# Kernel tuning notes

Hardware: AMD Instinct MI355X
Metric: run time of the kernel (lower is better)

Reference implementation:

```python
import jax, jax.numpy as jnp
import numpy as np

B, C, H, W = 16, 512, 64, 64
G = 32
CG = C // G       # per-group channels = 16


def setup_inputs() -> dict:
    key = jax.random.key(0)
    ks = jax.random.split(key, 6)
    def w(k, shape, fan_in):
        return (jax.random.normal(k, shape, jnp.float32) / np.float32(np.sqrt(fan_in)))
    return {
        "x": jax.random.normal(ks[0], (B, C, H, W), jnp.float32),
        "conv1_w": w(ks[1], (CG, CG), CG), "conv1_b": jnp.zeros((CG,), jnp.float32),
        "convh_w": w(ks[2], (CG, CG), CG), "convh_b": jnp.zeros((CG,), jnp.float32),
        "convw_w": w(ks[3], (CG, CG), CG), "convw_b": jnp.zeros((CG,), jnp.float32),
        "conv3_w": w(ks[4], (CG, CG, 3, 3), CG * 9), "conv3_b": jnp.zeros((CG,), jnp.float32),
        "gn_w": jnp.ones((CG,), jnp.float32), "gn_b": jnp.zeros((CG,), jnp.float32),
    }


def _conv1x1(y, w, b):
    # y: [N, Ci, L]  w: [Co, Ci]  -> [N, Co, L]
    return jnp.einsum('oi,bil->bol', w, y) + b[None, :, None]


def _ema_forward(x, conv1_w, conv1_b, convh_w, convh_b, convw_w, convw_b,
                 conv3_w, conv3_b, gn_w, gn_b):
    b, c, h, w = x.shape
    g, cg, hw = G, CG, h * w
    bg = b * g
    xg = x.reshape(bg, cg, h, w)

    # coordinate pooling: row means [bg,cg,h], col means [bg,cg,w]
    x_h = xg.mean(axis=3)                     # [bg, cg, h]
    x_w = xg.mean(axis=2)                     # [bg, cg, w]
    y = jnp.concatenate([x_h, x_w], axis=2)   # [bg, cg, h+w]
    y = jax.nn.relu(_conv1x1(y, conv1_w, conv1_b))
    y_h, y_w = y[:, :, :h], y[:, :, h:]

    a_h = jax.nn.sigmoid(_conv1x1(y_h, convh_w, convh_b))[:, :, :, None]  # [bg,cg,h,1]
    a_w = jax.nn.sigmoid(_conv1x1(y_w, convw_w, convw_b))[:, :, None, :]  # [bg,cg,1,w]

    x1 = xg * a_h * a_w

    # GroupNorm(num_groups=1): normalize over (cg,h,w) per sample, affine per channel
    mu = x1.mean(axis=(1, 2, 3), keepdims=True)
    var = ((x1 - mu) ** 2).mean(axis=(1, 2, 3), keepdims=True)
    x2 = (x1 - mu) * jax.lax.rsqrt(var + 1e-5)
    x2 = x2 * gn_w[None, :, None, None] + gn_b[None, :, None, None]

    # 3x3 conv branch
    x3 = jax.lax.conv_general_dilated(
        xg, conv3_w, window_strides=(1, 1), padding='SAME',
        dimension_numbers=('NCHW', 'OIHW', 'NCHW'))
    x3 = jax.nn.relu(x3 + conv3_b[None, :, None, None])

    A2 = jax.nn.softmax(x2.reshape(bg, cg, hw), axis=-1)  # [bg,cg,hw]
    A3 = jax.nn.softmax(x3.reshape(bg, cg, hw), axis=-1)
    V2 = x2.mean(axis=(2, 3))                              # [bg,cg]
    V3 = x3.mean(axis=(2, 3))

    s2 = jnp.einsum('bc,bcl->bl', V2, A3)  # [bg, hw]
    s3 = jnp.einsum('bc,bcl->bl', V3, A2)
    s = jax.nn.softmax(s2 + s3, axis=-1).reshape(bg, 1, h, w)

    return (xg * s).reshape(b, c, h, w)


def reference(x, conv1_w, conv1_b, convh_w, convh_b, convw_w, convw_b,
              conv3_w, conv3_b, gn_w, gn_b):
    return _ema_forward(x, conv1_w, conv1_b, convh_w, convh_b, convw_w, convw_b,
                        conv3_w, conv3_b, gn_w, gn_b)
```

## Files before the change

### kernel.cpp

```cpp
#include <hip/hip_runtime.h>
#include <hip/hip_bf16.h>

#define CHW  65536
#define CHW4 16384

__device__ __forceinline__ float wred(float v){
#pragma unroll
  for (int o = 32; o; o >>= 1) v += __shfl_xor(v, o, 64);
  return v;
}
__device__ __forceinline__ float wred16(float v){
#pragma unroll
  for (int o = 8; o; o >>= 1) v += __shfl_xor(v, o, 64);
  return v;
}
__device__ __forceinline__ float bf2f(unsigned short u){
  return __uint_as_float(((unsigned)u) << 16);
}

#define STR 84
__global__ __launch_bounds__(256, 6) void k3_conv(const float* __restrict__ x,
    const float* __restrict__ w3, const float* __restrict__ b3,
    __hip_bfloat16* __restrict__ E3,
    float* __restrict__ V3part, float* __restrict__ Z3part)
{
  __shared__ __align__(16) float in_s[8*10*STR];
  int tid = threadIdx.x;
  int s   = blockIdx.x;
  int bg  = blockIdx.y;
  size_t base  = (size_t)bg * CHW;
  const float4* x4 = (const float4*)x + (size_t)bg * CHW4;
  int lane = tid & 63;
  int cog = __builtin_amdgcn_readfirstlane(tid >> 6);
  int co0 = cog * 4;
  int r  = lane >> 3;
  int w0 = (lane & 7) * 8;
  float acc[4][8];
#pragma unroll
  for (int i = 0; i < 4; ++i)
#pragma unroll
    for (int px = 0; px < 8; ++px) acc[i][px] = 0.f;

#pragma unroll 1
  for (int half = 0; half < 2; ++half){
    __syncthreads();
    for (int idx = tid; idx < 1440; idx += 256){
      int q   = idx % 18;
      int rr  = (idx / 18) % 10;
      int ci8 = idx / 180;
      int hh  = s*8 - 1 + rr;
      float4 v = make_float4(0.f, 0.f, 0.f, 0.f);
      if (q >= 1 && q <= 16 && (unsigned)hh < 64u)
        v = x4[(half*8 + ci8)*1024 + hh*16 + (q-1)];
      *(float4*)&in_s[(ci8*10 + rr)*STR + q*4] = v;
    }
    __syncthreads();
#pragma unroll 1
    for (int ci8 = 0; ci8 < 8; ++ci8){
      int ci = half*8 + ci8;
      float wgt[4][9];
#pragma unroll
      for (int i = 0; i < 4; ++i)
#pragma unroll
        for (int t = 0; t < 9; ++t)
          wgt[i][t] = w3[((co0+i)*16 + ci)*9 + t];
#pragma unroll
      for (int dy = 0; dy < 3; ++dy){
        const float* row = &in_s[(ci8*10 + r + dy)*STR + w0];
        float4 A0 = *(const float4*)(row);
        float4 A1 = *(const float4*)(row+4);
        float4 A2v = *(const float4*)(row+8);
        float4 A3v = *(const float4*)(row+12);
        float v[16] = {A0.x,A0.y,A0.z,A0.w, A1.x,A1.y,A1.z,A1.w,
                       A2v.x,A2v.y,A2v.z,A2v.w, A3v.x,A3v.y,A3v.z,A3v.w};
#pragma unroll
        for (int dx = 0; dx < 3; ++dx){
#pragma unroll
          for (int px = 0; px < 8; ++px){
            float iv = v[px + dx + 3];
#pragma unroll
            for (int i = 0; i < 4; ++i)
              acc[i][px] = fmaf(wgt[i][dy*3+dx], iv, acc[i][px]);
          }
        }
      }
    }
  }
  int hh = s*8 + r;
#pragma unroll
  for (int i = 0; i < 4; ++i){
    float bias = b3[co0+i];
    union { __hip_bfloat16 hb[8]; uint4 u; } pk;
    float v3acc = 0.f, z3acc = 0.f;
#pragma unroll
    for (int px = 0; px < 8; ++px){
      float val = fmaxf(acc[i][px] + bias, 0.f);
      float e = __expf(val);
      v3acc += val;
      z3acc += e;
      pk.hb[px] = __float2bfloat16(e);
    }
    *(uint4*)&E3[base + (size_t)(co0+i)*4096 + hh*64 + w0] = pk.u;
    float rv = wred(v3acc);
    float rz = wred(z3acc);
    if (lane == 0){
      V3part[((size_t)bg*8 + s)*16 + co0 + i] = rv;
      Z3part[((size_t)bg*8 + s)*16 + co0 + i] = rz;
    }
  }
}

__global__ __launch_bounds__(1024, 8) void mega(const float* __restrict__ x,
    const float* __restrict__ w1, const float* __restrict__ b1,
    const float* __restrict__ wh, const float* __restrict__ bh,
    const float* __restrict__ ww, const float* __restrict__ bw,
    const float* __restrict__ gnw, const float* __restrict__ gnb,
    const float* __restrict__ V3part, const float* __restrict__ Z3part,
    const __hip_bfloat16* __restrict__ E3,
    float* __restrict__ out)
{
  __shared__ float rs[1024];
  __shared__ float cs[1024];
  __shared__ float ym[2048];
  __shared__ __align__(16) float ahs[1024], aws[1024];
  __shared__ float chpart[256], zpart[256];
  __shared__ float red1[16], red2[16];
  __shared__ float murs[2];
  __shared__ float sc_s[16], of_s[16], v2_s[16], p2s[16], p3s[16];
  __shared__ float invS_s;

  int tid = threadIdx.x, bg = blockIdx.x;
  const float4* x4 = (const float4*)x + (size_t)bg * CHW4;
  const ushort4* E34 = (const ushort4*)E3 + (size_t)bg * CHW4;
  float4* o4 = (float4*)out + (size_t)bg * CHW4;
  int h = tid >> 4, w4 = tid & 15, lane = tid & 63, wv = tid >> 6;

  cs[tid] = 0.f;
  __syncthreads();
#pragma unroll 4
  for (int k = 0; k < 16; ++k){
    float4 v = x4[k*1024 + tid];
    float srow = v.x + v.y + v.z + v.w;
    srow = wred16(srow);
    if ((tid & 15) == 0) rs[k*64 + h] = srow;
    v.x += __shfl_xor(v.x, 16); v.x += __shfl_xor(v.x, 32);
    v.y += __shfl_xor(v.y, 16); v.y += __shfl_xor(v.y, 32);
    v.z += __shfl_xor(v.z, 16); v.z += __shfl_xor(v.z, 32);
    v.w += __shfl_xor(v.w, 16); v.w += __shfl_xor(v.w, 32);
    if (lane < 16){
      atomicAdd(&cs[k*64 + lane*4 + 0], v.x);
      atomicAdd(&cs[k*64 + lane*4 + 1], v.y);
      atomicAdd(&cs[k*64 + lane*4 + 2], v.z);
      atomicAdd(&cs[k*64 + lane*4 + 3], v.w);
    }
  }
  __syncthreads();
  for (int ol = tid; ol < 2048; ol += 1024){
    int o = ol >> 7, l = ol & 127;
    float acc = b1[o];
#pragma unroll
    for (int i = 0; i < 16; ++i){
      float mv = (l < 64 ? rs[i*64 + l] : cs[i*64 + (l-64)]) * (1.f/64.f);
      acc = fmaf(w1[o*16 + i], mv, acc);
    }
    ym[o*128 + l] = fmaxf(acc, 0.f);
  }
  __syncthreads();
  for (int ol = tid; ol < 2048; ol += 1024){
    int q = ol >> 10;
    int o = (ol >> 6) & 15;
    int p = ol & 63;
    const float* Wm = q ? ww : wh;
    float acc = q ? bw[o] : bh[o];
#pragma unroll
    for (int i = 0; i < 16; ++i)
      acc = fmaf(Wm[o*16 + i], ym[i*128 + q*64 + p], acc);
    float sg = 1.f / (1.f + __expf(-acc));
    (q ? aws : ahs)[o*64 + p] = sg;
  }
  __syncthreads();

  const float4* aws4 = (const float4*)aws;
  float s1 = 0.f, s2 = 0.f;
#pragma unroll 4
  for (int k = 0; k < 16; ++k){
    float4 v = x4[k*1024 + tid];
    float ah = ahs[k*64 + h];
    float4 aw = aws4[k*16 + w4];
    float4 x1;
    x1.x = v.x * ah * aw.x;
    x1.y = v.y * ah * aw.y;
    x1.z = v.z * ah * aw.z;
    x1.w = v.w * ah * aw.w;
    float csum = x1.x + x1.y + x1.z + x1.w;
    s1 += csum;
    s2 = fmaf(x1.x, x1.x, s2); s2 = fmaf(x1.y, x1.y, s2);
    s2 = fmaf(x1.z, x1.z, s2); s2 = fmaf(x1.w, x1.w, s2);
    float cw = wred(csum);
    if (lane == 0) chpart[k*16 + wv] = cw;
  }
  float r1 = wred(s1), r2 = wred(s2);
  if (lane == 0){ red1[wv] = r1; red2[wv] = r2; }
  __syncthreads();
  if (tid == 0){
    float S = 0.f, SS = 0.f;
#pragma unroll
    for (int i = 0; i < 16; ++i){ S += red1[i]; SS += red2[i]; }
    float mu = S * (1.f/65536.f);
    float var = SS * (1.f/65536.f) - mu*mu;
    murs[0] = mu; murs[1] = rsqrtf(var + 1e-5f);
  }
  __syncthreads();
  if (tid < 16){
    float ch = 0.f;
#pragma unroll
    for (int m = 0; m < 16; ++m) ch += chpart[tid*16 + m];
    float mu = murs[0], rstd = murs[1];
    float g = gnw[tid], b = gnb[tid];
    float sc = rstd * g;
    sc_s[tid] = sc; of_s[tid] = b - mu*sc;
    v2_s[tid] = (ch * (1.f/4096.f) - mu) * sc + b;
  }
  __syncthreads();

#pragma unroll 2
  for (int k = 0; k < 16; ++k){
    float4 v = x4[k*1024 + tid];
    float ah = ahs[k*64 + h];
    float4 aw = aws4[k*16 + w4];
    float sc = sc_s[k], of = of_s[k];
    float z =  __expf(fmaf(v.x * ah * aw.x, sc, of));
    z += __expf(fmaf(v.y * ah * aw.y, sc, of));
    z += __expf(fmaf(v.z * ah * aw.z, sc, of));
    z += __expf(fmaf(v.w * ah * aw.w, sc, of));
    float zw = wred(z);
    if (lane == 0) zpart[k*16 + wv] = zw;
  }
  __syncthreads();
  if (tid < 16){
    float z2 = 0.f;
#pragma unroll
    for (int m = 0; m < 16; ++m) z2 += zpart[tid*16 + m];
    float v3 = 0.f, z3 = 0.f;
#pragma unroll
    for (int ss = 0; ss < 8; ++ss){
      v3 += V3part[((size_t)bg*8 + ss)*16 + tid];
      z3 += Z3part[((size_t)bg*8 + ss)*16 + tid];
    }
    p2s[tid] = v3 * (1.f/4096.f) / z2;
    p3s[tid] = v2_s[tid] / z3;
  }
  __syncthreads();

  float4 tacc = make_float4(0.f,0.f,0.f,0.f);
#pragma unroll 2
  for (int k = 0; k < 16; ++k){
    float4 v = x4[k*1024 + tid];
    ushort4 eu = E34[k*1024 + tid];
    float ah = ahs[k*64 + h];
    float4 aw = aws4[k*16 + w4];
    float sc = sc_s[k], of = of_s[k], p2 = p2s[k], p3 = p3s[k];
    tacc.x += __expf(fmaf(v.x*ah*aw.x, sc, of))*p2 + bf2f(eu.x)*p3;
    tacc.y += __expf(fmaf(v.y*ah*aw.y, sc, of))*p2 + bf2f(eu.y)*p3;
    tacc.z += __expf(fmaf(v.z*ah*aw.z, sc, of))*p2 + bf2f(eu.z)*p3;
    tacc.w += __expf(fmaf(v.w*ah*aw.w, sc, of))*p2 + bf2f(eu.w)*p3;
  }
  float4 e;
  e.x = __expf(tacc.x); e.y = __expf(tacc.y);
  e.z = __expf(tacc.z); e.w = __expf(tacc.w);
  float es = e.x + e.y + e.z + e.w;
  float rr = wred(es);
  if (lane == 0) red1[wv] = rr;
  __syncthreads();
  if (tid == 0){
    float S = 0.f;
#pragma unroll
    for (int i = 0; i < 16; ++i) S += red1[i];
    invS_s = 1.f / S;
  }
  __syncthreads();
  float iS = invS_s;
  float4 ei = make_float4(e.x*iS, e.y*iS, e.z*iS, e.w*iS);

#pragma unroll 4
  for (int k = 0; k < 16; ++k){
    float4 v = x4[k*1024 + tid];
    float4 ov;
    ov.x = v.x * ei.x; ov.y = v.y * ei.y;
    ov.z = v.z * ei.z; ov.w = v.w * ei.w;
    o4[k*1024 + tid] = ov;
  }
}

extern "C" void kernel_launch(void* const* d_in, const int* in_sizes, int n_in,
                              void* d_out, int out_size, void* d_ws, size_t ws_size,
                              hipStream_t stream)
{
  const float* x   = (const float*)d_in[0];
  const float* w1  = (const float*)d_in[1];
  const float* b1  = (const float*)d_in[2];
  const float* wh  = (const float*)d_in[3];
  const float* bh  = (const float*)d_in[4];
  const float* ww  = (const float*)d_in[5];
  const float* bw  = (const float*)d_in[6];
  const float* w3  = (const float*)d_in[7];
  const float* b3  = (const float*)d_in[8];
  const float* gnw = (const float*)d_in[9];
  const float* gnb = (const float*)d_in[10];
  float* out = (float*)d_out;

  float* V3part = (float*)d_ws;
  float* Z3part = V3part + 65536;
  __hip_bfloat16* E3 = (__hip_bfloat16*)(Z3part + 65536);
  (void)ws_size; (void)n_in; (void)in_sizes; (void)out_size;

  k3_conv<<<dim3(8, 512), 256, 0, stream>>>(x, w3, b3, E3, V3part, Z3part);
  mega   <<<512, 1024, 0, stream>>>(x, w1, b1, wh, bh, ww, bw, gnw, gnb,
                                    V3part, Z3part, E3, out);
}
```

Measured before the change: 470.3 us.

## Fuse 3x3 conv into main kernel, keep conv exponentials in shared memory

The separate conv kernel is merged into the per-group kernel. Four 256-thread units each compute two 8-row slabs of the 3x3 conv, prefetching the next slab's inputs into registers while computing the current one. Conv exponentials are stored as bf16 in LDS instead of a global workspace, and the GN-softmax exponentials are cached as packed bf16 in registers so the final pass does not recompute exp or reload x. This removes the global E3 round trip and one kernel launch. In exchange each block uses about 160KB of LDS, so only one block fits per CU, and the grid of 512 blocks gives reduced parallelism for the conv stage.

```diff
diff --git a/kernel.cpp b/kernel.cpp
--- a/kernel.cpp
+++ b/kernel.cpp
@@ -1,8 +1,8 @@
 #include <hip/hip_runtime.h>
 #include <hip/hip_bf16.h>
 
-#define CHW  65536
 #define CHW4 16384
+#define STR  84
 
 __device__ __forceinline__ float wred(float v){
 #pragma unroll
@@ -17,127 +17,159 @@
 __device__ __forceinline__ float bf2f(unsigned short u){
   return __uint_as_float(((unsigned)u) << 16);
 }
-
-#define STR 84
-__global__ __launch_bounds__(256, 6) void k3_conv(const float* __restrict__ x,
-    const float* __restrict__ w3, const float* __restrict__ b3,
-    __hip_bfloat16* __restrict__ E3,
-    float* __restrict__ V3part, float* __restrict__ Z3part)
-{
-  __shared__ __align__(16) float in_s[8*10*STR];
-  int tid = threadIdx.x;
-  int s   = blockIdx.x;
-  int bg  = blockIdx.y;
-  size_t base  = (size_t)bg * CHW;
-  const float4* x4 = (const float4*)x + (size_t)bg * CHW4;
-  int lane = tid & 63;
-  int cog = __builtin_amdgcn_readfirstlane(tid >> 6);
-  int co0 = cog * 4;
-  int r  = lane >> 3;
-  int w0 = (lane & 7) * 8;
-  float acc[4][8];
-#pragma unroll
-  for (int i = 0; i < 4; ++i)
-#pragma unroll
-    for (int px = 0; px < 8; ++px) acc[i][px] = 0.f;
-
-#pragma unroll 1
-  for (int half = 0; half < 2; ++half){
-    __syncthreads();
-    for (int idx = tid; idx < 1440; idx += 256){
-      int q   = idx % 18;
-      int rr  = (idx / 18) % 10;
-      int ci8 = idx / 180;
-      int hh  = s*8 - 1 + rr;
-      float4 v = make_float4(0.f, 0.f, 0.f, 0.f);
-      if (q >= 1 && q <= 16 && (unsigned)hh < 64u)
-        v = x4[(half*8 + ci8)*1024 + hh*16 + (q-1)];
-      *(float4*)&in_s[(ci8*10 + rr)*STR + q*4] = v;
-    }
-    __syncthreads();
-#pragma unroll 1
-    for (int ci8 = 0; ci8 < 8; ++ci8){
-      int ci = half*8 + ci8;
-      float wgt[4][9];
-#pragma unroll
-      for (int i = 0; i < 4; ++i)
-#pragma unroll
-        for (int t = 0; t < 9; ++t)
-          wgt[i][t] = w3[((co0+i)*16 + ci)*9 + t];
-#pragma unroll
-      for (int dy = 0; dy < 3; ++dy){
-        const float* row = &in_s[(ci8*10 + r + dy)*STR + w0];
-        float4 A0 = *(const float4*)(row);
-        float4 A1 = *(const float4*)(row+4);
-        float4 A2v = *(const float4*)(row+8);
-        float4 A3v = *(const float4*)(row+12);
-        float v[16] = {A0.x,A0.y,A0.z,A0.w, A1.x,A1.y,A1.z,A1.w,
-                       A2v.x,A2v.y,A2v.z,A2v.w, A3v.x,A3v.y,A3v.z,A3v.w};
-#pragma unroll
-        for (int dx = 0; dx < 3; ++dx){
-#pragma unroll
-          for (int px = 0; px < 8; ++px){
-            float iv = v[px + dx + 3];
-#pragma unroll
-            for (int i = 0; i < 4; ++i)
-              acc[i][px] = fmaf(wgt[i][dy*3+dx], iv, acc[i][px]);
-          }
-        }
-      }
-    }
-  }
-  int hh = s*8 + r;
-#pragma unroll
-  for (int i = 0; i < 4; ++i){
-    float bias = b3[co0+i];
-    union { __hip_bfloat16 hb[8]; uint4 u; } pk;
-    float v3acc = 0.f, z3acc = 0.f;
-#pragma unroll
-    for (int px = 0; px < 8; ++px){
-      float val = fmaxf(acc[i][px] + bias, 0.f);
-      float e = __expf(val);
-      v3acc += val;
-      z3acc += e;
-      pk.hb[px] = __float2bfloat16(e);
-    }
-    *(uint4*)&E3[base + (size_t)(co0+i)*4096 + hh*64 + w0] = pk.u;
-    float rv = wred(v3acc);
-    float rz = wred(z3acc);
-    if (lane == 0){
-      V3part[((size_t)bg*8 + s)*16 + co0 + i] = rv;
-      Z3part[((size_t)bg*8 + s)*16 + co0 + i] = rz;
-    }
-  }
-}
-
-__global__ __launch_bounds__(1024, 8) void mega(const float* __restrict__ x,
+__device__ __forceinline__ unsigned short f2b(float f){
+  union { __hip_bfloat16 h; unsigned short u; } cv;
+  cv.h = __float2bfloat16(f);
+  return cv.u;
+}
+
+__global__ __launch_bounds__(1024, 4) void ema_fused(const float* __restrict__ x,
     const float* __restrict__ w1, const float* __restrict__ b1,
     const float* __restrict__ wh, const float* __restrict__ bh,
     const float* __restrict__ ww, const float* __restrict__ bw,
+    const float* __restrict__ w3, const float* __restrict__ b3,
     const float* __restrict__ gnw, const float* __restrict__ gnb,
-    const float* __restrict__ V3part, const float* __restrict__ Z3part,
-    const __hip_bfloat16* __restrict__ E3,
     float* __restrict__ out)
 {
-  __shared__ float rs[1024];
-  __shared__ float cs[1024];
-  __shared__ float ym[2048];
-  __shared__ __align__(16) float ahs[1024], aws[1024];
+  __shared__ __align__(16) unsigned short E3s[16*4096];
+  __shared__ __align__(16) float uni[6720];
+  __shared__ float v3p[128], z3p[128];
   __shared__ float chpart[256], zpart[256];
   __shared__ float red1[16], red2[16];
   __shared__ float murs[2];
   __shared__ float sc_s[16], of_s[16], v2_s[16], p2s[16], p3s[16];
   __shared__ float invS_s;
 
-  int tid = threadIdx.x, bg = blockIdx.x;
+  const int tid = threadIdx.x;
+  const int bg  = blockIdx.x;
   const float4* x4 = (const float4*)x + (size_t)bg * CHW4;
-  const ushort4* E34 = (const ushort4*)E3 + (size_t)bg * CHW4;
   float4* o4 = (float4*)out + (size_t)bg * CHW4;
-  int h = tid >> 4, w4 = tid & 15, lane = tid & 63, wv = tid >> 6;
-
+
+  const int lane = tid & 63;
+  const int unit = __builtin_amdgcn_readfirstlane(tid >> 8);
+  const int ut   = tid & 255;
+  const int cog  = __builtin_amdgcn_readfirstlane((tid & 255) >> 6);
+  const int co0  = cog * 4;
+  const int cr   = lane >> 3;
+  const int w0   = (lane & 7) * 8;
+  float* in_u = &uni[unit * 1680];
+
+  const int q0  = ut % 18, rr0 = (ut / 18) % 10, c20 = ut / 180;
+  const int ut1 = ut + 256;
+  const int q1  = ut1 % 18, rr1 = (ut1 / 18) % 10, c21 = ut1 / 180;
+  const bool have1 = (ut < 104);
+
+  float acc[4][8];
+#pragma unroll
+  for (int i = 0; i < 4; ++i)
+#pragma unroll
+    for (int px = 0; px < 8; ++px) acc[i][px] = 0.f;
+
+  float4 pa, pb;
+  {
+    int hb = unit*16 - 1;
+    pa = make_float4(0.f,0.f,0.f,0.f); pb = make_float4(0.f,0.f,0.f,0.f);
+    int hh0 = hb + rr0;
+    if (q0 >= 1 && q0 <= 16 && (unsigned)hh0 < 64u)
+      pa = x4[c20*1024 + hh0*16 + (q0-1)];
+    if (have1){
+      int hh1 = hb + rr1;
+      if (q1 >= 1 && q1 <= 16 && (unsigned)hh1 < 64u)
+        pb = x4[c21*1024 + hh1*16 + (q1-1)];
+    }
+  }
+
+#pragma unroll 1
+  for (int round = 0; round < 16; ++round){
+    __syncthreads();
+    *(float4*)&in_u[(c20*10 + rr0)*STR + q0*4] = pa;
+    if (have1) *(float4*)&in_u[(c21*10 + rr1)*STR + q1*4] = pb;
+    __syncthreads();
+    if (round < 15){
+      int rn = round + 1;
+      int sg = unit*2 + (rn >> 3);
+      int cb = (rn & 7) * 2;
+      int hb = sg*8 - 1;
+      pa = make_float4(0.f,0.f,0.f,0.f); pb = make_float4(0.f,0.f,0.f,0.f);
+      int hh0 = hb + rr0;
+      if (q0 >= 1 && q0 <= 16 && (unsigned)hh0 < 64u)
+        pa = x4[(cb + c20)*1024 + hh0*16 + (q0-1)];
+      if (have1){
+        int hh1 = hb + rr1;
+        if (q1 >= 1 && q1 <= 16 && (unsigned)hh1 < 64u)
+          pb = x4[(cb + c21)*1024 + hh1*16 + (q1-1)];
+      }
+    }
+    const int ch2 = (round & 7) * 2;
+#pragma unroll
+    for (int c2 = 0; c2 < 2; ++c2){
+      const int ci = ch2 + c2;
+      float wgt[4][9];
+#pragma unroll
+      for (int i = 0; i < 4; ++i)
+#pragma unroll
+        for (int t = 0; t < 9; ++t)
+          wgt[i][t] = w3[((co0+i)*16 + ci)*9 + t];
+#pragma unroll
+      for (int dy = 0; dy < 3; ++dy){
+        const float* rowp = &in_u[(c2*10 + cr + dy)*STR + w0];
+        float4 A0  = *(const float4*)(rowp);
+        float4 A1  = *(const float4*)(rowp+4);
+        float4 A2v = *(const float4*)(rowp+8);
+        float4 A3v = *(const float4*)(rowp+12);
+        float v[16] = {A0.x,A0.y,A0.z,A0.w, A1.x,A1.y,A1.z,A1.w,
+                       A2v.x,A2v.y,A2v.z,A2v.w, A3v.x,A3v.y,A3v.z,A3v.w};
+#pragma unroll
+        for (int dx = 0; dx < 3; ++dx)
+#pragma unroll
+          for (int px = 0; px < 8; ++px){
+            float iv = v[px + dx + 3];
+#pragma unroll
+            for (int i = 0; i < 4; ++i)
+              acc[i][px] = fmaf(wgt[i][dy*3+dx], iv, acc[i][px]);
+          }
+      }
+    }
+    if ((round & 7) == 7){
+      const int sg = unit*2 + (round >> 3);
+      const int hh = sg*8 + cr;
+#pragma unroll
+      for (int i = 0; i < 4; ++i){
+        float bias = b3[co0+i];
+        union { unsigned short hb16[8]; uint4 u; } pk;
+        float v3acc = 0.f, z3acc = 0.f;
+#pragma unroll
+        for (int px = 0; px < 8; ++px){
+          float val = fmaxf(acc[i][px] + bias, 0.f);
+          float e = __expf(val);
+          v3acc += val; z3acc += e;
+          pk.hb16[px] = f2b(e);
+          acc[i][px] = 0.f;
+        }
+        *(uint4*)&E3s[(co0+i)*4096 + hh*64 + w0] = pk.u;
+        float rv = wred(v3acc);
+        float rz = wred(z3acc);
+        if (lane == 0){
+          v3p[sg*16 + co0 + i] = rv;
+          z3p[sg*16 + co0 + i] = rz;
+        }
+      }
+    }
+  }
+
+  float* rs  = uni;
+  float* cs  = uni + 1024;
+  float* ym  = uni + 2048;
+  float* ahs = uni + 4096;
+  float* aws = uni + 5120;
+  const int h   = tid >> 4;
+  const int w4i = tid & 15;
+  const int wv  = tid >> 6;
+
+  __syncthreads();
   cs[tid] = 0.f;
   __syncthreads();
-#pragma unroll 4
+#pragma unroll 8
   for (int k = 0; k < 16; ++k){
     float4 v = x4[k*1024 + tid];
     float srow = v.x + v.y + v.z + v.w;
@@ -157,13 +189,13 @@
   __syncthreads();
   for (int ol = tid; ol < 2048; ol += 1024){
     int o = ol >> 7, l = ol & 127;
-    float acc = b1[o];
+    float a = b1[o];
 #pragma unroll
     for (int i = 0; i < 16; ++i){
       float mv = (l < 64 ? rs[i*64 + l] : cs[i*64 + (l-64)]) * (1.f/64.f);
-      acc = fmaf(w1[o*16 + i], mv, acc);
-    }
-    ym[o*128 + l] = fmaxf(acc, 0.f);
+      a = fmaf(w1[o*16 + i], mv, a);
+    }
+    ym[o*128 + l] = fmaxf(a, 0.f);
   }
   __syncthreads();
   for (int ol = tid; ol < 2048; ol += 1024){
@@ -171,22 +203,22 @@
     int o = (ol >> 6) & 15;
     int p = ol & 63;
     const float* Wm = q ? ww : wh;
-    float acc = q ? bw[o] : bh[o];
+    float a = q ? bw[o] : bh[o];
 #pragma unroll
     for (int i = 0; i < 16; ++i)
-      acc = fmaf(Wm[o*16 + i], ym[i*128 + q*64 + p], acc);
-    float sg = 1.f / (1.f + __expf(-acc));
-    (q ? aws : ahs)[o*64 + p] = sg;
+      a = fmaf(Wm[o*16 + i], ym[i*128 + q*64 + p], a);
+    float sgm = 1.f / (1.f + __expf(-a));
+    (q ? aws : ahs)[o*64 + p] = sgm;
   }
   __syncthreads();
 
   const float4* aws4 = (const float4*)aws;
   float s1 = 0.f, s2 = 0.f;
-#pragma unroll 4
+#pragma unroll 8
   for (int k = 0; k < 16; ++k){
     float4 v = x4[k*1024 + tid];
     float ah = ahs[k*64 + h];
-    float4 aw = aws4[k*16 + w4];
+    float4 aw = aws4[k*16 + w4i];
     float4 x1;
     x1.x = v.x * ah * aw.x;
     x1.y = v.y * ah * aw.y;
@@ -206,7 +238,7 @@
     float S = 0.f, SS = 0.f;
 #pragma unroll
     for (int i = 0; i < 16; ++i){ S += red1[i]; SS += red2[i]; }
-    float mu = S * (1.f/65536.f);
+    float mu  = S * (1.f/65536.f);
     float var = SS * (1.f/65536.f) - mu*mu;
     murs[0] = mu; murs[1] = rsqrtf(var + 1e-5f);
   }
@@ -223,16 +255,20 @@
   }
   __syncthreads();
 
-#pragma unroll 2
+  unsigned e2a[16], e2b[16];
+#pragma unroll
   for (int k = 0; k < 16; ++k){
     float4 v = x4[k*1024 + tid];
     float ah = ahs[k*64 + h];
-    float4 aw = aws4[k*16 + w4];
+    float4 aw = aws4[k*16 + w4i];
     float sc = sc_s[k], of = of_s[k];
-    float z =  __expf(fmaf(v.x * ah * aw.x, sc, of));
-    z += __expf(fmaf(v.y * ah * aw.y, sc, of));
-    z += __expf(fmaf(v.z * ah * aw.z, sc, of));
-    z += __expf(fmaf(v.w * ah * aw.w, sc, of));
+    float ex = __expf(fmaf(v.x * ah * aw.x, sc, of));
+    float ey = __expf(fmaf(v.y * ah * aw.y, sc, of));
+    float ez = __expf(fmaf(v.z * ah * aw.z, sc, of));
+    float ew = __expf(fmaf(v.w * ah * aw.w, sc, of));
+    float z = ex + ey + ez + ew;
+    e2a[k] = (unsigned)f2b(ex) | ((unsigned)f2b(ey) << 16);
+    e2b[k] = (unsigned)f2b(ez) | ((unsigned)f2b(ew) << 16);
     float zw = wred(z);
     if (lane == 0) zpart[k*16 + wv] = zw;
   }
@@ -244,8 +280,8 @@
     float v3 = 0.f, z3 = 0.f;
 #pragma unroll
     for (int ss = 0; ss < 8; ++ss){
-      v3 += V3part[((size_t)bg*8 + ss)*16 + tid];
-      z3 += Z3part[((size_t)bg*8 + ss)*16 + tid];
+      v3 += v3p[ss*16 + tid];
+      z3 += z3p[ss*16 + tid];
     }
     p2s[tid] = v3 * (1.f/4096.f) / z2;
     p3s[tid] = v2_s[tid] / z3;
@@ -253,17 +289,14 @@
   __syncthreads();
 
   float4 tacc = make_float4(0.f,0.f,0.f,0.f);
-#pragma unroll 2
-  for (int k = 0; k < 16; ++k){
-    float4 v = x4[k*1024 + tid];
-    ushort4 eu = E34[k*1024 + tid];
-    float ah = ahs[k*64 + h];
-    float4 aw = aws4[k*16 + w4];
-    float sc = sc_s[k], of = of_s[k], p2 = p2s[k], p3 = p3s[k];
-    tacc.x += __expf(fmaf(v.x*ah*aw.x, sc, of))*p2 + bf2f(eu.x)*p3;
-    tacc.y += __expf(fmaf(v.y*ah*aw.y, sc, of))*p2 + bf2f(eu.y)*p3;
-    tacc.z += __expf(fmaf(v.z*ah*aw.z, sc, of))*p2 + bf2f(eu.z)*p3;
-    tacc.w += __expf(fmaf(v.w*ah*aw.w, sc, of))*p2 + bf2f(eu.w)*p3;
+#pragma unroll
+  for (int k = 0; k < 16; ++k){
+    ushort4 eu = *(const ushort4*)&E3s[k*4096 + tid*4];
+    float p2 = p2s[k], p3 = p3s[k];
+    tacc.x += bf2f((unsigned short)(e2a[k] & 0xffffu))*p2 + bf2f(eu.x)*p3;
+    tacc.y += bf2f((unsigned short)(e2a[k] >> 16))   *p2 + bf2f(eu.y)*p3;
+    tacc.z += bf2f((unsigned short)(e2b[k] & 0xffffu))*p2 + bf2f(eu.z)*p3;
+    tacc.w += bf2f((unsigned short)(e2b[k] >> 16))   *p2 + bf2f(eu.w)*p3;
   }
   float4 e;
   e.x = __expf(tacc.x); e.y = __expf(tacc.y);
@@ -282,7 +315,7 @@
   float iS = invS_s;
   float4 ei = make_float4(e.x*iS, e.y*iS, e.z*iS, e.w*iS);
 
-#pragma unroll 4
+#pragma unroll 8
   for (int k = 0; k < 16; ++k){
     float4 v = x4[k*1024 + tid];
     float4 ov;
@@ -308,13 +341,8 @@
   const float* gnw = (const float*)d_in[9];
   const float* gnb = (const float*)d_in[10];
   float* out = (float*)d_out;
-
-  float* V3part = (float*)d_ws;
-  float* Z3part = V3part + 65536;
-  __hip_bfloat16* E3 = (__hip_bfloat16*)(Z3part + 65536);
-  (void)ws_size; (void)n_in; (void)in_sizes; (void)out_size;
-
-  k3_conv<<<dim3(8, 512), 256, 0, stream>>>(x, w3, b3, E3, V3part, Z3part);
-  mega   <<<512, 1024, 0, stream>>>(x, w1, b1, wh, bh, ww, bw, gnw, gnb,
-                                    V3part, Z3part, E3, out);
-}
+  (void)d_ws; (void)ws_size; (void)n_in; (void)in_sizes; (void)out_size;
+
+  ema_fused<<<dim3(512), 1024, 0, stream>>>(x, w1, b1, wh, bh, ww, bw,
+                                            w3, b3, gnw, gnb, out);
+}
```

Measured after the change: 542.8 us. 15.4% more time.

## Fuse pooling into conv kernel, cache exp in registers, reorder shared-memory layout

Applied to the files above, without the earlier changes.

The conv kernel now computes row sums and per-strip column partial sums from its shared-memory tile and writes them to workspace, so the mega kernel no longer makes a full pass over x for pooling. The conv kernel's shared tile uses a narrower stride with even/odd float4 slot interleaving, which is meant to reduce bank conflicts. The mega kernel stores the GroupNorm-softmax exponentials as packed bf16 in registers during the Z-sum pass and reuses them in the final pass, removing one read of x and the recomputed exps. In exchange it adds extra workspace traffic for the column partials, more register pressure, and bf16 rounding of the A2 exponentials.

```diff
diff --git a/kernel.cpp b/kernel.cpp
--- a/kernel.cpp
+++ b/kernel.cpp
@@ -3,6 +3,7 @@
 
 #define CHW  65536
 #define CHW4 16384
+#define KSTR 72
 
 __device__ __forceinline__ float wred(float v){
 #pragma unroll
@@ -17,16 +18,21 @@
 __device__ __forceinline__ float bf2f(unsigned short u){
   return __uint_as_float(((unsigned)u) << 16);
 }
-
-#define STR 84
+__device__ __forceinline__ unsigned short f2b(float f){
+  union { __hip_bfloat16 h; unsigned short u; } cv;
+  cv.h = __float2bfloat16(f);
+  return cv.u;
+}
+
 __global__ __launch_bounds__(256, 6) void k3_conv(const float* __restrict__ x,
     const float* __restrict__ w3, const float* __restrict__ b3,
     __hip_bfloat16* __restrict__ E3,
-    float* __restrict__ V3part, float* __restrict__ Z3part)
+    float* __restrict__ V3part, float* __restrict__ Z3part,
+    float* __restrict__ rs_g, float* __restrict__ csp_g)
 {
-  __shared__ __align__(16) float in_s[8*10*STR];
+  __shared__ __align__(16) float in_s[8*10*KSTR];
   int tid = threadIdx.x;
-  int s   = blockIdx.x;
+  int st  = blockIdx.x;
   int bg  = blockIdx.y;
   size_t base  = (size_t)bg * CHW;
   const float4* x4 = (const float4*)x + (size_t)bg * CHW4;
@@ -34,7 +40,7 @@
   int cog = __builtin_amdgcn_readfirstlane(tid >> 6);
   int co0 = cog * 4;
   int r  = lane >> 3;
-  int w0 = (lane & 7) * 8;
+  int cc = lane & 7;
   float acc[4][8];
 #pragma unroll
   for (int i = 0; i < 4; ++i)
@@ -45,16 +51,50 @@
   for (int half = 0; half < 2; ++half){
     __syncthreads();
     for (int idx = tid; idx < 1440; idx += 256){
-      int q   = idx % 18;
+      int p   = idx % 18;
       int rr  = (idx / 18) % 10;
       int ci8 = idx / 180;
-      int hh  = s*8 - 1 + rr;
+      int sl  = (p <= 8) ? 2*p : 2*(p-9)+1;
+      int hh  = st*8 - 1 + rr;
       float4 v = make_float4(0.f, 0.f, 0.f, 0.f);
-      if (q >= 1 && q <= 16 && (unsigned)hh < 64u)
-        v = x4[(half*8 + ci8)*1024 + hh*16 + (q-1)];
-      *(float4*)&in_s[(ci8*10 + rr)*STR + q*4] = v;
+      if (sl >= 1 && sl <= 16 && (unsigned)hh < 64u)
+        v = x4[(half*8 + ci8)*1024 + hh*16 + (sl-1)];
+      *(float4*)&in_s[(ci8*10 + rr)*KSTR + p*4] = v;
     }
     __syncthreads();
+
+    {
+      int task = tid >> 2, sub = tid & 3;
+      int pci = task >> 3, prow = task & 7;
+      const float* rowp = &in_s[(pci*10 + 1 + prow)*KSTR];
+      float4 a  = *(const float4*)(rowp + 4*(2*sub+9));
+      float4 b  = *(const float4*)(rowp + 4*(2*sub+1));
+      float4 cf = *(const float4*)(rowp + 4*(2*sub+10));
+      float4 d  = *(const float4*)(rowp + 4*(2*sub+2));
+      float sm = a.x+a.y+a.z+a.w + b.x+b.y+b.z+b.w
+               + cf.x+cf.y+cf.z+cf.w + d.x+d.y+d.z+d.w;
+      sm += __shfl_xor(sm, 1, 64);
+      sm += __shfl_xor(sm, 2, 64);
+      if (sub == 0)
+        rs_g[(size_t)bg*1024 + (half*8 + pci)*64 + st*8 + prow] = sm;
+    }
+    {
+      int pci = tid >> 5;
+      int c0  = (tid & 31) * 2;
+#pragma unroll
+      for (int e = 0; e < 2; ++e){
+        int c  = c0 + e;
+        int sl = (c >> 2) + 1;
+        int pp = (sl >> 1) + 9*(sl & 1);
+        int dd = pp*4 + (c & 3);
+        float a2 = 0.f;
+#pragma unroll
+        for (int rr2 = 0; rr2 < 8; ++rr2)
+          a2 += in_s[(pci*10 + 1 + rr2)*KSTR + dd];
+        csp_g[((size_t)(bg*8 + st)*16 + half*8 + pci)*64 + c] = a2;
+      }
+    }
+
 #pragma unroll 1
     for (int ci8 = 0; ci8 < 8; ++ci8){
       int ci = half*8 + ci8;
@@ -66,11 +106,11 @@
           wgt[i][t] = w3[((co0+i)*16 + ci)*9 + t];
 #pragma unroll
       for (int dy = 0; dy < 3; ++dy){
-        const float* row = &in_s[(ci8*10 + r + dy)*STR + w0];
-        float4 A0 = *(const float4*)(row);
-        float4 A1 = *(const float4*)(row+4);
-        float4 A2v = *(const float4*)(row+8);
-        float4 A3v = *(const float4*)(row+12);
+        const float* rowp = &in_s[(ci8*10 + r + dy)*KSTR];
+        float4 A0  = *(const float4*)(rowp + 4*cc);
+        float4 A1  = *(const float4*)(rowp + 4*(cc+9));
+        float4 A2v = *(const float4*)(rowp + 4*(cc+1));
+        float4 A3v = *(const float4*)(rowp + 4*(cc+10));
         float v[16] = {A0.x,A0.y,A0.z,A0.w, A1.x,A1.y,A1.z,A1.w,
                        A2v.x,A2v.y,A2v.z,A2v.w, A3v.x,A3v.y,A3v.z,A3v.w};
 #pragma unroll
@@ -86,11 +126,11 @@
       }
     }
   }
-  int hh = s*8 + r;
+  int hh = st*8 + r;
 #pragma unroll
   for (int i = 0; i < 4; ++i){
     float bias = b3[co0+i];
-    union { __hip_bfloat16 hb[8]; uint4 u; } pk;
+    union { unsigned short hb[8]; uint4 u; } pk;
     float v3acc = 0.f, z3acc = 0.f;
 #pragma unroll
     for (int px = 0; px < 8; ++px){
@@ -98,14 +138,14 @@
       float e = __expf(val);
       v3acc += val;
       z3acc += e;
-      pk.hb[px] = __float2bfloat16(e);
-    }
-    *(uint4*)&E3[base + (size_t)(co0+i)*4096 + hh*64 + w0] = pk.u;
+      pk.hb[px] = f2b(e);
+    }
+    *(uint4*)&E3[base + (size_t)(co0+i)*4096 + hh*64 + cc*8] = pk.u;
     float rv = wred(v3acc);
     float rz = wred(z3acc);
     if (lane == 0){
-      V3part[((size_t)bg*8 + s)*16 + co0 + i] = rv;
-      Z3part[((size_t)bg*8 + s)*16 + co0 + i] = rz;
+      V3part[((size_t)bg*8 + st)*16 + co0 + i] = rv;
+      Z3part[((size_t)bg*8 + st)*16 + co0 + i] = rz;
     }
   }
 }
@@ -116,6 +156,7 @@
     const float* __restrict__ ww, const float* __restrict__ bw,
     const float* __restrict__ gnw, const float* __restrict__ gnb,
     const float* __restrict__ V3part, const float* __restrict__ Z3part,
+    const float* __restrict__ rs_g, const float* __restrict__ csp_g,
     const __hip_bfloat16* __restrict__ E3,
     float* __restrict__ out)
 {
@@ -135,24 +176,13 @@
   float4* o4 = (float4*)out + (size_t)bg * CHW4;
   int h = tid >> 4, w4 = tid & 15, lane = tid & 63, wv = tid >> 6;
 
-  cs[tid] = 0.f;
-  __syncthreads();
-#pragma unroll 4
-  for (int k = 0; k < 16; ++k){
-    float4 v = x4[k*1024 + tid];
-    float srow = v.x + v.y + v.z + v.w;
-    srow = wred16(srow);
-    if ((tid & 15) == 0) rs[k*64 + h] = srow;
-    v.x += __shfl_xor(v.x, 16); v.x += __shfl_xor(v.x, 32);
-    v.y += __shfl_xor(v.y, 16); v.y += __shfl_xor(v.y, 32);
-    v.z += __shfl_xor(v.z, 16); v.z += __shfl_xor(v.z, 32);
-    v.w += __shfl_xor(v.w, 16); v.w += __shfl_xor(v.w, 32);
-    if (lane < 16){
-      atomicAdd(&cs[k*64 + lane*4 + 0], v.x);
-      atomicAdd(&cs[k*64 + lane*4 + 1], v.y);
-      atomicAdd(&cs[k*64 + lane*4 + 2], v.z);
-      atomicAdd(&cs[k*64 + lane*4 + 3], v.w);
-    }
+  rs[tid] = rs_g[(size_t)bg*1024 + tid];
+  {
+    const float* cp = csp_g + (size_t)bg*8192;
+    float csum = 0.f;
+#pragma unroll
+    for (int ss = 0; ss < 8; ++ss) csum += cp[ss*1024 + tid];
+    cs[tid] = csum;
   }
   __syncthreads();
   for (int ol = tid; ol < 2048; ol += 1024){
@@ -223,16 +253,20 @@
   }
   __syncthreads();
 
+  unsigned e2a[16], e2b[16];
 #pragma unroll 2
   for (int k = 0; k < 16; ++k){
     float4 v = x4[k*1024 + tid];
     float ah = ahs[k*64 + h];
     float4 aw = aws4[k*16 + w4];
     float sc = sc_s[k], of = of_s[k];
-    float z =  __expf(fmaf(v.x * ah * aw.x, sc, of));
-    z += __expf(fmaf(v.y * ah * aw.y, sc, of));
-    z += __expf(fmaf(v.z * ah * aw.z, sc, of));
-    z += __expf(fmaf(v.w * ah * aw.w, sc, of));
+    float ex = __expf(fmaf(v.x * ah * aw.x, sc, of));
+    float ey = __expf(fmaf(v.y * ah * aw.y, sc, of));
+    float ez = __expf(fmaf(v.z * ah * aw.z, sc, of));
+    float ew = __expf(fmaf(v.w * ah * aw.w, sc, of));
+    float z = ex + ey + ez + ew;
+    e2a[k] = (unsigned)f2b(ex) | ((unsigned)f2b(ey) << 16);
+    e2b[k] = (unsigned)f2b(ez) | ((unsigned)f2b(ew) << 16);
     float zw = wred(z);
     if (lane == 0) zpart[k*16 + wv] = zw;
   }
@@ -253,17 +287,14 @@
   __syncthreads();
 
   float4 tacc = make_float4(0.f,0.f,0.f,0.f);
-#pragma unroll 2
+#pragma unroll 4
   for (int k = 0; k < 16; ++k){
-    float4 v = x4[k*1024 + tid];
     ushort4 eu = E34[k*1024 + tid];
-    float ah = ahs[k*64 + h];
-    float4 aw = aws4[k*16 + w4];
-    float sc = sc_s[k], of = of_s[k], p2 = p2s[k], p3 = p3s[k];
-    tacc.x += __expf(fmaf(v.x*ah*aw.x, sc, of))*p2 + bf2f(eu.x)*p3;
-    tacc.y += __expf(fmaf(v.y*ah*aw.y, sc, of))*p2 + bf2f(eu.y)*p3;
-    tacc.z += __expf(fmaf(v.z*ah*aw.z, sc, of))*p2 + bf2f(eu.z)*p3;
-    tacc.w += __expf(fmaf(v.w*ah*aw.w, sc, of))*p2 + bf2f(eu.w)*p3;
+    float p2 = p2s[k], p3 = p3s[k];
+    tacc.x += bf2f((unsigned short)(e2a[k] & 0xffffu))*p2 + bf2f(eu.x)*p3;
+    tacc.y += bf2f((unsigned short)(e2a[k] >> 16))   *p2 + bf2f(eu.y)*p3;
+    tacc.z += bf2f((unsigned short)(e2b[k] & 0xffffu))*p2 + bf2f(eu.z)*p3;
+    tacc.w += bf2f((unsigned short)(e2b[k] >> 16))   *p2 + bf2f(eu.w)*p3;
   }
   float4 e;
   e.x = __expf(tacc.x); e.y = __expf(tacc.y);
@@ -311,10 +342,13 @@
 
   float* V3part = (float*)d_ws;
   float* Z3part = V3part + 65536;
-  __hip_bfloat16* E3 = (__hip_bfloat16*)(Z3part + 65536);
+  float* rs_g   = Z3part + 65536;
+  float* csp_g  = rs_g + 524288;
+  __hip_bfloat16* E3 = (__hip_bfloat16*)(csp_g + 4194304);
   (void)ws_size; (void)n_in; (void)in_sizes; (void)out_size;
 
-  k3_conv<<<dim3(8, 512), 256, 0, stream>>>(x, w3, b3, E3, V3part, Z3part);
+  k3_conv<<<dim3(8, 512), 256, 0, stream>>>(x, w3, b3, E3, V3part, Z3part,
+                                            rs_g, csp_g);
   mega   <<<512, 1024, 0, stream>>>(x, w1, b1, wh, bh, ww, bw, gnw, gnb,
-                                    V3part, Z3part, E3, out);
-}
+                                    V3part, Z3part, rs_g, csp_g, E3, out);
+}
```

New measurement: 452.4 us. -3.8%, faster.
